# Kernel optimization log

Hardware: AMD Instinct MI355X
Metric: run time of the kernel (lower is better)

## Reference

```python
import jax, jax.numpy as jnp
import numpy as np

N_NODES = 100000
N_EDGES = 1000000
HID = 128


def setup_inputs() -> dict:
    key = jax.random.key(0)
    ks = jax.random.split(key, 6)
    x = jax.random.normal(ks[0], (N_NODES, HID), dtype=jnp.float32)
    edge_index = jax.random.randint(ks[1], (2, N_EDGES), 0, N_NODES, dtype=jnp.int32)
    edge_attr = jax.random.uniform(ks[2], (N_EDGES, 1), dtype=jnp.float32)
    # MLP params (PyTorch Linear default-ish init scale)
    d_in = 2 * HID + 1  # 257
    W1 = jax.random.normal(ks[3], (d_in, HID), dtype=jnp.float32) / np.sqrt(d_in)
    b1 = jnp.zeros((HID,), dtype=jnp.float32)
    W2 = jax.random.normal(ks[4], (HID, 32), dtype=jnp.float32) / np.sqrt(HID)
    b2 = jnp.zeros((32,), dtype=jnp.float32)
    W3 = jax.random.normal(ks[5], (32, 1), dtype=jnp.float32) / np.sqrt(32.0)
    b3 = jnp.zeros((1,), dtype=jnp.float32)
    return {"x": x, "edge_index": edge_index, "edge_attr": edge_attr,
            "W1": W1, "b1": b1, "W2": W2, "b2": b2, "W3": W3, "b3": b3}


def reference(x, edge_index, edge_attr, W1, b1, W2, b2, W3, b3):
    src = edge_index[0]
    dst = edge_index[1]
    # [E, 2*H+1] gather + concat
    ef = jnp.concatenate([x[src], x[dst], edge_attr], axis=1)
    h = jax.nn.relu(ef @ W1 + b1)          # [E, H] (dropout = identity in eval)
    h = jax.nn.relu(h @ W2 + b2)           # [E, 32]
    out = jax.nn.sigmoid(h @ W3 + b3)      # [E, 1]
    return out[:, 0]                        # [E]
```

## Files before the change

### kernel.cpp

```cpp
#include <hip/hip_runtime.h>

#define E_EDGES 1000000
#define NNODES  100000
#define HID     128
#define NG      31250
#define NBLK    768
#define NT      62500
#define EBLK    768

typedef float f32x4 __attribute__((ext_vector_type(4)));
typedef short s16x8 __attribute__((ext_vector_type(8)));

typedef __attribute__((address_space(3))) unsigned int lds_u32;
typedef const __attribute__((address_space(1))) unsigned int glb_u32;

__device__ __forceinline__ void gl_lds16(const void* g, void* l) {
  __builtin_amdgcn_global_load_lds((glb_u32*)g, (lds_u32*)l, 16, 0, 0);
}

__device__ __forceinline__ unsigned short f2bf(float f) {
  unsigned int u = __float_as_uint(f);
  u += 0x7FFFu + ((u >> 16) & 1u);
  return (unsigned short)(u >> 16);
}

__device__ __forceinline__ unsigned int cvtpk_bf16(float lo, float hi) {
  unsigned int r;
  asm("v_cvt_pk_bf16_f32 %0, %1, %2" : "=v"(r) : "v"(lo), "v"(hi));
  return r;
}

__device__ __forceinline__ float bflo(unsigned int u) {
  return __uint_as_float(u << 16);
}
__device__ __forceinline__ float bfhi(unsigned int u) {
  return __uint_as_float(u & 0xffff0000u);
}

__device__ __forceinline__ int4 pack8(float4 a, float4 b) {
  int4 v;
  v.x = (int)((unsigned)f2bf(a.x) | ((unsigned)f2bf(a.y) << 16));
  v.y = (int)((unsigned)f2bf(a.z) | ((unsigned)f2bf(a.w) << 16));
  v.z = (int)((unsigned)f2bf(b.x) | ((unsigned)f2bf(b.y) << 16));
  v.w = (int)((unsigned)f2bf(b.z) | ((unsigned)f2bf(b.w) << 16));
  return v;
}

__global__ void cast_x_kernel(const float* __restrict__ x,
                              unsigned short* __restrict__ xb) {
  int i = blockIdx.x * blockDim.x + threadIdx.x;
  const float4* p = (const float4*)x;
  float4 a = p[2 * i];
  float4 b = p[2 * i + 1];
  int4 v = pack8(a, b);
  ((int4*)xb)[i] = v;
}

__global__ void edge_naive(const float* __restrict__ x, const int* __restrict__ ei,
                           const float* __restrict__ attr, const float* __restrict__ W1,
                           const float* __restrict__ b1, const float* __restrict__ W2,
                           const float* __restrict__ b2, const float* __restrict__ W3,
                           const float* __restrict__ b3, float* __restrict__ out) {
  const int e = blockIdx.x * blockDim.x + threadIdx.x;
  if (e >= E_EDGES) return;
  const float* xs = x + (size_t)ei[e] * HID;
  const float* xd = x + (size_t)ei[E_EDGES + e] * HID;
  const float a = attr[e];
  float h1[HID];
  for (int n = 0; n < HID; ++n) {
    float s = b1[n] + a * W1[256 * HID + n];
    for (int k = 0; k < HID; ++k)
      s += xs[k] * W1[k * HID + n] + xd[k] * W1[(128 + k) * HID + n];
    h1[n] = fmaxf(s, 0.f);
  }
  float o = b3[0];
  for (int n2 = 0; n2 < 32; ++n2) {
    float s = b2[n2];
    for (int n = 0; n < HID; ++n) s += h1[n] * W2[n * 32 + n2];
    o += fmaxf(s, 0.f) * W3[n2];
  }
  out[e] = 1.f / (1.f + __expf(-o));
}

__launch_bounds__(256, 3)
__global__ void edge_mlp_kernel(const unsigned short* __restrict__ xb,
                                const int* __restrict__ ei,
                                const float* __restrict__ attr,
                                const float* __restrict__ W1,
                                const float* __restrict__ b1,
                                const float* __restrict__ W2,
                                const float* __restrict__ b2,
                                const float* __restrict__ W3,
                                const float* __restrict__ b3,
                                float* __restrict__ out) {
  __shared__ __align__(16) unsigned char ef[2][16384];
  __shared__ __align__(16) unsigned char h1b[2][8704];
  __shared__ float red[2][4][16];

  const int tid  = threadIdx.x;
  const int w    = tid >> 6;
  const int lane = tid & 63;
  const int q    = lane >> 4;
  const int l15  = lane & 15;

  s16x8 B1[2][8];
  float b1v[2], w1l[2];
#pragma unroll
  for (int th = 0; th < 2; ++th) {
    const int nc = w * 32 + th * 16 + l15;
#pragma unroll
    for (int s = 0; s < 8; ++s)
#pragma unroll
      for (int j = 0; j < 8; ++j)
        B1[th][s][j] = (short)f2bf(W1[(s * 32 + q * 8 + j) * HID + nc]);
    b1v[th] = b1[nc];
    w1l[th] = W1[256 * HID + nc];
  }
  const int n2 = (w & 1) * 16 + l15;
  s16x8 B2[4];
#pragma unroll
  for (int s2 = 0; s2 < 4; ++s2)
#pragma unroll
    for (int j = 0; j < 8; ++j) {
      const int e = s2 * 32 + q * 8 + j;
      const int n = (e >> 5) * 32 + (e & 1) * 16 + ((e >> 1) & 15);
      B2[s2][j] = (short)f2bf(W2[n * 32 + n2]);
    }
  const float b2v = b2[n2];
  const float w3v = W3[n2];
  const float b3v = b3[0];

  const int bx = blockIdx.x;
  int nidA[4] = {0, 0, 0, 0}, nidB[4] = {0, 0, 0, 0};
  const int itmax = (NG - 1 - bx) / NBLK + 2;

  {
#pragma unroll
    for (int i = 0; i < 4; ++i) {
      const int f = w * 4 + i;
      nidA[i] = ei[(f >> 3) * E_EDGES + bx * 32 + (f & 7) * 4 + q];
    }
#pragma unroll
    for (int i = 0; i < 4; ++i) {
      const int f = w * 4 + i, m = (f & 7) * 4 + q;
      gl_lds16(xb + (size_t)nidA[i] * HID + ((l15 ^ (m & 7)) << 3),
               &ef[0][f * 1024]);
    }
    const int g1 = bx + NBLK;
    if (g1 < NG) {
#pragma unroll
      for (int i = 0; i < 4; ++i) {
        const int f = w * 4 + i;
        nidB[i] = ei[(f >> 3) * E_EDGES + g1 * 32 + (f & 7) * 4 + q];
      }
    }
  }
  __syncthreads();

#define ITER(IT, P, NIDU, NIDL)                                               \
  {                                                                           \
    const int g   = bx + (IT) * NBLK;                                         \
    const int g1  = g + NBLK;                                                 \
    const int g2  = g + 2 * NBLK;                                             \
    const int gm1 = g - NBLK;                                                 \
    const int gm2 = g - 2 * NBLK;                                             \
    if (g1 < NG) {                                                            \
      _Pragma("unroll") for (int i = 0; i < 4; ++i) {                         \
        const int f = w * 4 + i, m = (f & 7) * 4 + q;                         \
        gl_lds16(xb + (size_t)NIDU[i] * HID + ((l15 ^ (m & 7)) << 3),         \
                 &ef[(P) ^ 1][f * 1024]);                                     \
      }                                                                       \
    }                                                                         \
    if (g2 < NG) {                                                            \
      _Pragma("unroll") for (int i = 0; i < 4; ++i) {                         \
        const int f = w * 4 + i;                                              \
        NIDL[i] = ei[(f >> 3) * E_EDGES + g2 * 32 + (f & 7) * 4 + q];         \
      }                                                                       \
    }                                                                         \
    if (g < NG) {                                                             \
      const f32x4 at0 = *(const f32x4*)(attr + g * 32 + q * 4);               \
      const f32x4 at1 = *(const f32x4*)(attr + g * 32 + 16 + q * 4);          \
      _Pragma("unroll") for (int t = 0; t < 2; ++t) {                         \
        f32x4 a0 = {0.f, 0.f, 0.f, 0.f}, a1 = {0.f, 0.f, 0.f, 0.f};          \
        _Pragma("unroll") for (int s = 0; s < 8; ++s) {                       \
          const int ch = s * 4 + q;                                           \
          const s16x8 A = *(const s16x8*)&ef[P][(ch >> 4) * 8192 + t * 4096   \
              + l15 * 256 + (((ch & 15) ^ (l15 & 7)) << 4)];                  \
          a0 = __builtin_amdgcn_mfma_f32_16x16x32_bf16(A, B1[0][s], a0, 0, 0, 0); \
          a1 = __builtin_amdgcn_mfma_f32_16x16x32_bf16(A, B1[1][s], a1, 0, 0, 0); \
        }                                                                     \
        const f32x4 at = t ? at1 : at0;                                       \
        _Pragma("unroll") for (int r = 0; r < 4; ++r) {                       \
          const float v0 = fmaxf(a0[r] + b1v[0] + at[r] * w1l[0], 0.f);       \
          const float v1 = fmaxf(a1[r] + b1v[1] + at[r] * w1l[1], 0.f);       \
          const unsigned int pk =                                             \
              (unsigned)f2bf(v0) | ((unsigned)f2bf(v1) << 16);                \
          *(unsigned int*)&h1b[P][t * 4352 + (q * 4 + r) * 272                \
                                  + (w * 16 + l15) * 4] = pk;                 \
        }                                                                     \
      }                                                                       \
    }                                                                         \
    if (gm1 >= 0 && gm1 < NG) {                                               \
      const int t = w >> 1;                                                   \
      f32x4 c0 = {0.f, 0.f, 0.f, 0.f};                                        \
      _Pragma("unroll") for (int s2 = 0; s2 < 4; ++s2) {                      \
        const s16x8 A2 = *(const s16x8*)&h1b[(P) ^ 1][t * 4352 + l15 * 272    \
                                                      + s2 * 64 + q * 16];    \
        c0 = __builtin_amdgcn_mfma_f32_16x16x32_bf16(A2, B2[s2], c0, 0, 0, 0); \
      }                                                                       \
      float p0 = fmaxf(c0[0] + b2v, 0.f) * w3v;                               \
      float p1 = fmaxf(c0[1] + b2v, 0.f) * w3v;                               \
      float p2 = fmaxf(c0[2] + b2v, 0.f) * w3v;                               \
      float p3 = fmaxf(c0[3] + b2v, 0.f) * w3v;                               \
      _Pragma("unroll") for (int off = 8; off >= 1; off >>= 1) {              \
        p0 += __shfl_xor(p0, off, 16);                                        \
        p1 += __shfl_xor(p1, off, 16);                                        \
        p2 += __shfl_xor(p2, off, 16);                                        \
        p3 += __shfl_xor(p3, off, 16);                                        \
      }                                                                       \
      if (l15 == 0) {                                                         \
        red[P][w][q * 4 + 0] = p0;                                            \
        red[P][w][q * 4 + 1] = p1;                                            \
        red[P][w][q * 4 + 2] = p2;                                            \
        red[P][w][q * 4 + 3] = p3;                                            \
      }                                                                       \
    }                                                                         \
    if (gm2 >= 0 && tid < 32) {                                               \
      const int tt = tid >> 4, mm = tid & 15;                                 \
      const float sv = red[(P) ^ 1][tt * 2][mm]                               \
                     + red[(P) ^ 1][tt * 2 + 1][mm] + b3v;                    \
      out[gm2 * 32 + tid] = 1.f / (1.f + __expf(-sv));                        \
    }                                                                         \
    __syncthreads();                                                          \
  }

  for (int itb = 0;; itb += 2) {
    ITER(itb, 0, nidB, nidA)
    if (itb >= itmax) break;
    ITER(itb + 1, 1, nidA, nidB)
    if (itb + 1 >= itmax) break;
  }
#undef ITER
}

__global__ void node_precompute(const float* __restrict__ x,
                                const float* __restrict__ W1,
                                const float* __restrict__ b1,
                                unsigned short* __restrict__ Pa,
                                unsigned short* __restrict__ Pb) {
  __shared__ __align__(16) unsigned char xs[32 * 272];
  const int tid = threadIdx.x;
  const int w = tid >> 6, lane = tid & 63, q = lane >> 4, l15 = lane & 15;
  const int n0 = blockIdx.x * 32;

  {
    const int r = tid >> 3, cc = tid & 7;
    const float* src = x + (size_t)(n0 + r) * HID + cc * 16;
    float4 f0 = ((const float4*)src)[0];
    float4 f1 = ((const float4*)src)[1];
    float4 f2 = ((const float4*)src)[2];
    float4 f3 = ((const float4*)src)[3];
    *(int4*)&xs[r * 272 + cc * 32]      = pack8(f0, f1);
    *(int4*)&xs[r * 272 + cc * 32 + 16] = pack8(f2, f3);
  }
  __syncthreads();

  s16x8 Bf[4][4];
  float bh[4];
  int sides[4], ncols[4];
#pragma unroll
  for (int nt = 0; nt < 4; ++nt) {
    const int c = w * 64 + nt * 16 + l15;
    const int side = c >> 7, n = c & 127;
    sides[nt] = side; ncols[nt] = n;
    bh[nt] = 0.5f * b1[n];
#pragma unroll
    for (int s = 0; s < 4; ++s)
#pragma unroll
      for (int j = 0; j < 8; ++j)
        Bf[nt][s][j] = (short)f2bf(W1[(side * 128 + s * 32 + q * 8 + j) * HID + n]);
  }

#pragma unroll
  for (int mt = 0; mt < 2; ++mt) {
    s16x8 A[4];
#pragma unroll
    for (int s = 0; s < 4; ++s)
      A[s] = *(const s16x8*)&xs[(mt * 16 + l15) * 272 + (s * 4 + q) * 16];
#pragma unroll
    for (int nt = 0; nt < 4; ++nt) {
      f32x4 acc = {0.f, 0.f, 0.f, 0.f};
#pragma unroll
      for (int s = 0; s < 4; ++s)
        acc = __builtin_amdgcn_mfma_f32_16x16x32_bf16(A[s], Bf[nt][s], acc, 0, 0, 0);
      unsigned short* dst = sides[nt] ? Pb : Pa;
#pragma unroll
      for (int r = 0; r < 4; ++r) {
        const int node = n0 + mt * 16 + q * 4 + r;
        dst[(size_t)node * HID + ncols[nt]] = f2bf(acc[r] + bh[nt]);
      }
    }
  }
}

__launch_bounds__(256, 3)
__global__ void edge_mlp2(const unsigned short* __restrict__ Pa,
                          const unsigned short* __restrict__ Pb,
                          const int* __restrict__ ei,
                          const float* __restrict__ attr,
                          const float* __restrict__ W1,
                          const float* __restrict__ W2,
                          const float* __restrict__ b2,
                          const float* __restrict__ W3,
                          const float* __restrict__ b3,
                          float* __restrict__ out) {
  const int tid = threadIdx.x;
  const int w = tid >> 6, lane = tid & 63, q = lane >> 4, l15 = lane & 15;
  const int wid = blockIdx.x * 4 + w;
  const int nw  = EBLK * 4;

  s16x8 B2a[4], B2b[4];
#pragma unroll
  for (int s = 0; s < 4; ++s)
#pragma unroll
    for (int j = 0; j < 8; ++j) {
      const int k = s * 32 + q * 8 + j;
      B2a[s][j] = (short)f2bf(W2[k * 32 + l15]);
      B2b[s][j] = (short)f2bf(W2[k * 32 + 16 + l15]);
    }
  int4 w1p[4];
#pragma unroll
  for (int s = 0; s < 4; ++s) {
    unsigned int uu[4];
#pragma unroll
    for (int m = 0; m < 4; ++m) {
      const int k = s * 32 + q * 8 + 2 * m;
      uu[m] = (unsigned)f2bf(W1[256 * HID + k]) |
              ((unsigned)f2bf(W1[256 * HID + k + 1]) << 16);
    }
    w1p[s] = make_int4((int)uu[0], (int)uu[1], (int)uu[2], (int)uu[3]);
  }
  const float b2a = b2[l15], b2b = b2[16 + l15];
  const float w3a = W3[l15], w3b = W3[16 + l15];
  const float b3v = b3[0];

  int t = wid;
  if (t >= NT) return;
  int sid = ei[t * 16 + l15];
  int did = ei[E_EDGES + t * 16 + l15];
  float at = attr[t * 16 + l15];

  while (true) {
    const unsigned short* pa = Pa + (size_t)sid * HID;
    const unsigned short* pb = Pb + (size_t)did * HID;
    int4 ga[4], gb[4];
#pragma unroll
    for (int s = 0; s < 4; ++s)
      ga[s] = *(const int4*)((const char*)pa + s * 64 + q * 16);
#pragma unroll
    for (int s = 0; s < 4; ++s)
      gb[s] = *(const int4*)((const char*)pb + s * 64 + q * 16);

    const int tn = t + nw;
    int sid2 = 0, did2 = 0;
    float at2 = 0.f;
    if (tn < NT) {
      sid2 = ei[tn * 16 + l15];
      did2 = ei[E_EDGES + tn * 16 + l15];
      at2  = attr[tn * 16 + l15];
    }

    f32x4 c0 = {0.f, 0.f, 0.f, 0.f}, c1 = {0.f, 0.f, 0.f, 0.f};
    const float atv = at;
#pragma unroll
    for (int s = 0; s < 4; ++s) {
      const unsigned int* ua = (const unsigned int*)&ga[s];
      const unsigned int* ub = (const unsigned int*)&gb[s];
      const unsigned int* uw = (const unsigned int*)&w1p[s];
      int4 afi;
      unsigned int* af = (unsigned int*)&afi;
#pragma unroll
      for (int m = 0; m < 4; ++m) {
        float v0 = bflo(ua[m]) + bflo(ub[m]) + atv * bflo(uw[m]);
        float v1 = bfhi(ua[m]) + bfhi(ub[m]) + atv * bfhi(uw[m]);
        v0 = fmaxf(v0, 0.f);
        v1 = fmaxf(v1, 0.f);
        af[m] = cvtpk_bf16(v0, v1);
      }
      const s16x8 A = *(const s16x8*)&afi;
      c0 = __builtin_amdgcn_mfma_f32_16x16x32_bf16(A, B2a[s], c0, 0, 0, 0);
      c1 = __builtin_amdgcn_mfma_f32_16x16x32_bf16(A, B2b[s], c1, 0, 0, 0);
    }

    float p0 = fmaxf(c0[0] + b2a, 0.f) * w3a + fmaxf(c1[0] + b2b, 0.f) * w3b;
    float p1 = fmaxf(c0[1] + b2a, 0.f) * w3a + fmaxf(c1[1] + b2b, 0.f) * w3b;
    float p2 = fmaxf(c0[2] + b2a, 0.f) * w3a + fmaxf(c1[2] + b2b, 0.f) * w3b;
    float p3 = fmaxf(c0[3] + b2a, 0.f) * w3a + fmaxf(c1[3] + b2b, 0.f) * w3b;
#pragma unroll
    for (int off = 8; off >= 1; off >>= 1) {
      p0 += __shfl_xor(p0, off, 16);
      p1 += __shfl_xor(p1, off, 16);
      p2 += __shfl_xor(p2, off, 16);
      p3 += __shfl_xor(p3, off, 16);
    }
    if (l15 == 0) {
      float4 o4;
      o4.x = 1.f / (1.f + __expf(-(p0 + b3v)));
      o4.y = 1.f / (1.f + __expf(-(p1 + b3v)));
      o4.z = 1.f / (1.f + __expf(-(p2 + b3v)));
      o4.w = 1.f / (1.f + __expf(-(p3 + b3v)));
      *(float4*)&out[t * 16 + q * 4] = o4;
    }

    if (tn >= NT) break;
    t = tn; sid = sid2; did = did2; at = at2;
  }
}

extern "C" void kernel_launch(void* const* d_in, const int* in_sizes, int n_in,
                              void* d_out, int out_size, void* d_ws, size_t ws_size,
                              hipStream_t stream) {
  const float* x    = (const float*)d_in[0];
  const int*   ei   = (const int*)d_in[1];
  const float* attr = (const float*)d_in[2];
  const float* W1   = (const float*)d_in[3];
  const float* b1   = (const float*)d_in[4];
  const float* W2   = (const float*)d_in[5];
  const float* b2   = (const float*)d_in[6];
  const float* W3   = (const float*)d_in[7];
  const float* b3   = (const float*)d_in[8];
  float* out = (float*)d_out;

  const size_t needP = (size_t)NNODES * HID * 2 * sizeof(unsigned short);
  const size_t need1 = (size_t)NNODES * HID * sizeof(unsigned short);
  if (ws_size >= needP) {
    unsigned short* Pa = (unsigned short*)d_ws;
    unsigned short* Pb = Pa + (size_t)NNODES * HID;
    node_precompute<<<NNODES / 32, 256, 0, stream>>>(x, W1, b1, Pa, Pb);
    edge_mlp2<<<EBLK, 256, 0, stream>>>(Pa, Pb, ei, attr, W1, W2, b2, W3, b3, out);
  } else if (ws_size >= need1) {
    unsigned short* xb = (unsigned short*)d_ws;
    cast_x_kernel<<<6250, 256, 0, stream>>>(x, xb);
    edge_mlp_kernel<<<NBLK, 256, 0, stream>>>(xb, ei, attr, W1, b1, W2, b2, W3, b3, out);
  } else {
    edge_naive<<<(E_EDGES + 255) / 256, 256, 0, stream>>>(x, ei, attr, W1, b1, W2, b2, W3, b3, out);
  }
}
```

Baseline: 205.8 us.

## Persistent node precompute with packed bf16 stores, permuted layout, more edge blocks

The node precompute kernel becomes persistent: each block loads its W1 fragment once and loops over node tiles. It now writes packed pairs of bf16 values as 32-bit stores in a permuted column order instead of scattered 16-bit stores. The edge kernel's W2 and W1-attr fragments are permuted to match the new layout. The edge grid doubles and the launch bounds target 6 waves per SIMD instead of 3, which may force register spills.

```diff
diff --git a/kernel.cpp b/kernel.cpp
--- a/kernel.cpp
+++ b/kernel.cpp
@@ -6,7 +6,8 @@
 #define NG      31250
 #define NBLK    768
 #define NT      62500
-#define EBLK    768
+#define EBLK    1536
+#define PBLK    512
 
 typedef float f32x4 __attribute__((ext_vector_type(4)));
 typedef short s16x8 __attribute__((ext_vector_type(8)));
@@ -243,69 +244,77 @@
 #undef ITER
 }
 
+__launch_bounds__(256, 2)
 __global__ void node_precompute(const float* __restrict__ x,
                                 const float* __restrict__ W1,
                                 const float* __restrict__ b1,
-                                unsigned short* __restrict__ Pa,
-                                unsigned short* __restrict__ Pb) {
+                                unsigned int* __restrict__ Pa,
+                                unsigned int* __restrict__ Pb) {
   __shared__ __align__(16) unsigned char xs[32 * 272];
   const int tid = threadIdx.x;
   const int w = tid >> 6, lane = tid & 63, q = lane >> 4, l15 = lane & 15;
-  const int n0 = blockIdx.x * 32;
-
-  {
-    const int r = tid >> 3, cc = tid & 7;
-    const float* src = x + (size_t)(n0 + r) * HID + cc * 16;
-    float4 f0 = ((const float4*)src)[0];
-    float4 f1 = ((const float4*)src)[1];
-    float4 f2 = ((const float4*)src)[2];
-    float4 f3 = ((const float4*)src)[3];
-    *(int4*)&xs[r * 272 + cc * 32]      = pack8(f0, f1);
-    *(int4*)&xs[r * 272 + cc * 32 + 16] = pack8(f2, f3);
-  }
-  __syncthreads();
+  const int side = w >> 1;
+  const int cb   = (w & 1) * 64;
 
   s16x8 Bf[4][4];
   float bh[4];
-  int sides[4], ncols[4];
 #pragma unroll
   for (int nt = 0; nt < 4; ++nt) {
-    const int c = w * 64 + nt * 16 + l15;
-    const int side = c >> 7, n = c & 127;
-    sides[nt] = side; ncols[nt] = n;
-    bh[nt] = 0.5f * b1[n];
+    const int c = cb + nt * 16 + l15;
+    bh[nt] = 0.5f * b1[c];
 #pragma unroll
     for (int s = 0; s < 4; ++s)
 #pragma unroll
       for (int j = 0; j < 8; ++j)
-        Bf[nt][s][j] = (short)f2bf(W1[(side * 128 + s * 32 + q * 8 + j) * HID + n]);
-  }
-
-#pragma unroll
-  for (int mt = 0; mt < 2; ++mt) {
-    s16x8 A[4];
-#pragma unroll
-    for (int s = 0; s < 4; ++s)
-      A[s] = *(const s16x8*)&xs[(mt * 16 + l15) * 272 + (s * 4 + q) * 16];
-#pragma unroll
-    for (int nt = 0; nt < 4; ++nt) {
-      f32x4 acc = {0.f, 0.f, 0.f, 0.f};
+        Bf[nt][s][j] = (short)f2bf(W1[(side * 128 + s * 32 + q * 8 + j) * HID + c]);
+  }
+  unsigned int* const dstP = side ? Pb : Pa;
+
+  for (int tile = blockIdx.x; tile < NNODES / 32; tile += gridDim.x) {
+    const int n0 = tile * 32;
+    {
+      const int r = tid >> 3, cc = tid & 7;
+      const float* src = x + (size_t)(n0 + r) * HID + cc * 16;
+      float4 f0 = ((const float4*)src)[0];
+      float4 f1 = ((const float4*)src)[1];
+      float4 f2 = ((const float4*)src)[2];
+      float4 f3 = ((const float4*)src)[3];
+      *(int4*)&xs[r * 272 + cc * 32]      = pack8(f0, f1);
+      *(int4*)&xs[r * 272 + cc * 32 + 16] = pack8(f2, f3);
+    }
+    __syncthreads();
+
+#pragma unroll
+    for (int mt = 0; mt < 2; ++mt) {
+      s16x8 A[4];
 #pragma unroll
       for (int s = 0; s < 4; ++s)
-        acc = __builtin_amdgcn_mfma_f32_16x16x32_bf16(A[s], Bf[nt][s], acc, 0, 0, 0);
-      unsigned short* dst = sides[nt] ? Pb : Pa;
-#pragma unroll
-      for (int r = 0; r < 4; ++r) {
-        const int node = n0 + mt * 16 + q * 4 + r;
-        dst[(size_t)node * HID + ncols[nt]] = f2bf(acc[r] + bh[nt]);
+        A[s] = *(const s16x8*)&xs[(mt * 16 + l15) * 272 + (s * 4 + q) * 16];
+      f32x4 acc[4];
+#pragma unroll
+      for (int nt = 0; nt < 4; ++nt) {
+        acc[nt] = (f32x4){0.f, 0.f, 0.f, 0.f};
+#pragma unroll
+        for (int s = 0; s < 4; ++s)
+          acc[nt] = __builtin_amdgcn_mfma_f32_16x16x32_bf16(A[s], Bf[nt][s], acc[nt], 0, 0, 0);
       }
-    }
-  }
-}
-
-__launch_bounds__(256, 3)
-__global__ void edge_mlp2(const unsigned short* __restrict__ Pa,
-                          const unsigned short* __restrict__ Pb,
+#pragma unroll
+      for (int p = 0; p < 2; ++p)
+#pragma unroll
+        for (int r = 0; r < 4; ++r) {
+          const int node = n0 + mt * 16 + q * 4 + r;
+          const unsigned int pk = cvtpk_bf16(acc[2 * p][r] + bh[2 * p],
+                                             acc[2 * p + 1][r] + bh[2 * p + 1]);
+          dstP[(size_t)node * 64 + (w & 1) * 32 + p * 16 + l15] = pk;
+        }
+    }
+    __syncthreads();
+  }
+}
+
+__launch_bounds__(256, 6)
+__global__ void edge_mlp2(const unsigned int* __restrict__ Pa,
+                          const unsigned int* __restrict__ Pb,
                           const int* __restrict__ ei,
                           const float* __restrict__ attr,
                           const float* __restrict__ W1,
@@ -324,9 +333,9 @@
   for (int s = 0; s < 4; ++s)
 #pragma unroll
     for (int j = 0; j < 8; ++j) {
-      const int k = s * 32 + q * 8 + j;
-      B2a[s][j] = (short)f2bf(W2[k * 32 + l15]);
-      B2b[s][j] = (short)f2bf(W2[k * 32 + 16 + l15]);
+      const int n = s * 32 + q * 4 + (j >> 1) + ((j & 1) << 4);
+      B2a[s][j] = (short)f2bf(W2[n * 32 + l15]);
+      B2b[s][j] = (short)f2bf(W2[n * 32 + 16 + l15]);
     }
   int4 w1p[4];
 #pragma unroll
@@ -334,9 +343,9 @@
     unsigned int uu[4];
 #pragma unroll
     for (int m = 0; m < 4; ++m) {
-      const int k = s * 32 + q * 8 + 2 * m;
-      uu[m] = (unsigned)f2bf(W1[256 * HID + k]) |
-              ((unsigned)f2bf(W1[256 * HID + k + 1]) << 16);
+      const int n = s * 32 + q * 4 + m;
+      uu[m] = (unsigned)f2bf(W1[256 * HID + n]) |
+              ((unsigned)f2bf(W1[256 * HID + n + 16]) << 16);
     }
     w1p[s] = make_int4((int)uu[0], (int)uu[1], (int)uu[2], (int)uu[3]);
   }
@@ -351,15 +360,15 @@
   float at = attr[t * 16 + l15];
 
   while (true) {
-    const unsigned short* pa = Pa + (size_t)sid * HID;
-    const unsigned short* pb = Pb + (size_t)did * HID;
+    const unsigned int* pa = Pa + (size_t)sid * 64;
+    const unsigned int* pb = Pb + (size_t)did * 64;
     int4 ga[4], gb[4];
 #pragma unroll
     for (int s = 0; s < 4; ++s)
-      ga[s] = *(const int4*)((const char*)pa + s * 64 + q * 16);
+      ga[s] = *(const int4*)(pa + s * 16 + q * 4);
 #pragma unroll
     for (int s = 0; s < 4; ++s)
-      gb[s] = *(const int4*)((const char*)pb + s * 64 + q * 16);
+      gb[s] = *(const int4*)(pb + s * 16 + q * 4);
 
     const int tn = t + nw;
     int sid2 = 0, did2 = 0;
@@ -434,9 +443,9 @@
   const size_t needP = (size_t)NNODES * HID * 2 * sizeof(unsigned short);
   const size_t need1 = (size_t)NNODES * HID * sizeof(unsigned short);
   if (ws_size >= needP) {
-    unsigned short* Pa = (unsigned short*)d_ws;
-    unsigned short* Pb = Pa + (size_t)NNODES * HID;
-    node_precompute<<<NNODES / 32, 256, 0, stream>>>(x, W1, b1, Pa, Pb);
+    unsigned int* Pa = (unsigned int*)d_ws;
+    unsigned int* Pb = Pa + (size_t)NNODES * 64;
+    node_precompute<<<PBLK, 256, 0, stream>>>(x, W1, b1, Pa, Pb);
     edge_mlp2<<<EBLK, 256, 0, stream>>>(Pa, Pb, ei, attr, W1, W2, b2, W3, b3, out);
   } else if (ws_size >= need1) {
     unsigned short* xb = (unsigned short*)d_ws;
```

New measurement: 294.8 us. 1.43x slower.
